# Performance work log

Measured on AMD Instinct MI355X. Metric: run time of the kernel, lower is better.

## Reference

```python
import jax, jax.numpy as jnp
import numpy as np

B, N, K = 4, 4096, 16
DP, DM = 64, 128
EPS = 1e-8


def setup_inputs() -> dict:
    key = jax.random.key(0)
    ks = jax.random.split(key, 32)
    g = lambda i, shape, fan: jax.random.normal(ks[i], shape, jnp.float32) / np.sqrt(fan)
    inp = {
        'xyz': jax.random.normal(ks[0], (B, N, 3), jnp.float32),
        'features': jax.random.normal(ks[1], (B, N, DP), jnp.float32),
        # fc1: d_points -> d_model
        'fc1_w': g(2, (DP, DM), DP), 'fc1_b': jnp.zeros((DM,), jnp.float32),
        # fc2: d_model -> d_points
        'fc2_w': g(3, (DM, DP), DM), 'fc2_b': jnp.zeros((DP,), jnp.float32),
        # fc_delta: Linear(3,DM) -> ReLU -> Linear(DM,DM)
        'd1_w': g(4, (3, DM), 3), 'd1_b': jnp.zeros((DM,), jnp.float32),
        'd2_w': g(5, (DM, DM), DM), 'd2_b': jnp.zeros((DM,), jnp.float32),
        # fc_gamma: Linear(DM,DM) -> ReLU -> Linear(DM,DM)
        'g1_w': g(6, (DM, DM), DM), 'g1_b': jnp.zeros((DM,), jnp.float32),
        'g2_w': g(7, (DM, DM), DM), 'g2_b': jnp.zeros((DM,), jnp.float32),
        # q/k/v projections, no bias
        'wq_w': g(8, (DM, DM), DM), 'wk_w': g(9, (DM, DM), DM), 'wv_w': g(10, (DM, DM), DM),
        # fc_sim: Linear(DM+1, DM)
        'sim_w': g(11, (DM + 1, DM), DM + 1), 'sim_b': jnp.zeros((DM,), jnp.float32),
    }
    return inp


def _gather(t, idx):
    # t: [B, N, C], idx: [B, N, K] -> [B, N, K, C]
    bidx = jnp.arange(t.shape[0])[:, None, None]
    return t[bidx, idx]


def reference(xyz, features, fc1_w, fc1_b, fc2_w, fc2_b, d1_w, d1_b, d2_w, d2_b,
              g1_w, g1_b, g2_w, g2_b, wq_w, wk_w, wv_w, sim_w, sim_b):
    # pairwise squared distances [B, N, N]
    sq = jnp.sum(xyz * xyz, axis=-1)
    dists = sq[:, :, None] + sq[:, None, :] - 2.0 * jnp.einsum('bnc,bmc->bnm', xyz, xyz)
    knn_idx = jnp.argsort(dists, axis=-1)[:, :, :K]            # [B, N, K]

    knn_xyz = _gather(xyz, knn_idx)                            # [B, N, K, 3]
    x = features @ fc1_w + fc1_b                               # [B, N, DM]
    q = x @ wq_w                                               # [B, N, DM]
    k = _gather(x @ wk_w, knn_idx)                             # [B, N, K, DM]
    v = _gather(x @ wv_w, knn_idx)                             # [B, N, K, DM]

    rel_pos = xyz[:, :, None, :] - knn_xyz                     # [B, N, K, 3]
    pos_enc = jax.nn.relu(rel_pos @ d1_w + d1_b) @ d2_w + d2_b # [B, N, K, DM]

    qe = q[:, :, None, :]                                      # [B, N, 1, DM]
    # torch cosine_similarity: dot / (max(||q||,eps) * max(||k||,eps))
    qn = jnp.maximum(jnp.linalg.norm(q, axis=-1), EPS)[:, :, None]
    kn = jnp.maximum(jnp.linalg.norm(k, axis=-1), EPS)
    sim = jnp.sum(qe * k, axis=-1) / (qn * kn)                 # [B, N, K]

    rel_qk = jnp.concatenate([sim[..., None], qe - k], axis=-1)  # [B, N, K, DM+1]
    rel_qk = rel_qk @ sim_w + sim_b                            # [B, N, K, DM]

    attn = jax.nn.relu((rel_qk + pos_enc) @ g1_w + g1_b) @ g2_w + g2_b
    attn = jax.nn.softmax(attn / np.sqrt(DM).astype(np.float32), axis=-2)  # over K

    res = jnp.einsum('bnkf,bnkf->bnf', attn, v + pos_enc)      # [B, N, DM]
    res = res @ fc2_w + fc2_b + features                       # [B, N, DP]
    return res, attn
```

## Files before the change

kernel.cpp:

```cpp
#include <hip/hip_runtime.h>
#include <hip/hip_bf16.h>

#define BB 4
#define NN 4096
#define KK 16
#define DP 64
#define DM 128
#define DMP 132
#define EPSF 1e-8f
#define OUT0N ((size_t)BB * NN * DP)

typedef unsigned short u16t;
typedef __attribute__((ext_vector_type(8))) short s8v;
typedef __attribute__((ext_vector_type(4))) float f4v;

__device__ int g_flag;

__device__ __forceinline__ float u2f(u16t u) {
    unsigned int x = ((unsigned int)u) << 16;
    return __uint_as_float(x);
}
__device__ __forceinline__ u16t f2u(float v) {
    __hip_bfloat16 h = __float2bfloat16(v);
    return *(u16t*)&h;
}

template<int DT> struct IO;
template<> struct IO<0> {
    static __device__ __forceinline__ float ld(const void* p, size_t i) { return ((const float*)p)[i]; }
    static __device__ __forceinline__ void ld4(const void* p, size_t i, float o[4]) {
        float4 v = *(const float4*)((const float*)p + i);
        o[0] = v.x; o[1] = v.y; o[2] = v.z; o[3] = v.w;
    }
    static __device__ __forceinline__ void st(void* p, size_t i, float v) { ((float*)p)[i] = v; }
};
template<> struct IO<1> {
    static __device__ __forceinline__ float ld(const void* p, size_t i) { return u2f(((const u16t*)p)[i]); }
    static __device__ __forceinline__ void ld4(const void* p, size_t i, float o[4]) {
        ushort4 v = *(const ushort4*)((const u16t*)p + i);
        o[0] = u2f(v.x); o[1] = u2f(v.y); o[2] = u2f(v.z); o[3] = u2f(v.w);
    }
    static __device__ __forceinline__ void st(void* p, size_t i, float v) { ((u16t*)p)[i] = f2u(v); }
};

__global__ __launch_bounds__(64) void detect_kernel(const void* feat) {
    const int tid = threadIdx.x;
    float x = u2f(((const u16t*)feat)[2 * tid]);
    float a = fabsf(x);
    bool sane = (x == 0.0f) || (a > 1e-4f && a < 50.0f);
    unsigned long long m = __ballot(sane);
    if (tid == 0) g_flag = (__popcll(m) >= 32) ? 1 : 0;
}

struct QkvSmem { float sf[DP]; float sx[DM]; };

template<int DT>
__device__ __forceinline__ void qkv_body(QkvSmem& s,
    const void* feat, const void* fc1_w, const void* fc1_b,
    const void* wq, const void* wk, const void* wv,
    float* __restrict__ qbuf, float* __restrict__ kbuf, float* __restrict__ vbuf)
{
    const int bn = blockIdx.x;
    const int tid = threadIdx.x;
    if (tid < DP) s.sf[tid] = IO<DT>::ld(feat, (size_t)bn * DP + tid);
    __syncthreads();
    float x = IO<DT>::ld(fc1_b, tid);
#pragma unroll 4
    for (int i = 0; i < DP; i++) x = fmaf(s.sf[i], IO<DT>::ld(fc1_w, i * DM + tid), x);
    s.sx[tid] = x;
    __syncthreads();
    float q = 0.f, k = 0.f, v = 0.f;
    for (int i0 = 0; i0 < DM; i0 += 4) {
        float4 xv = *(const float4*)&s.sx[i0];
        const float xs[4] = { xv.x, xv.y, xv.z, xv.w };
#pragma unroll
        for (int j = 0; j < 4; j++) {
            q = fmaf(xs[j], IO<DT>::ld(wq, (i0 + j) * DM + tid), q);
            k = fmaf(xs[j], IO<DT>::ld(wk, (i0 + j) * DM + tid), k);
            v = fmaf(xs[j], IO<DT>::ld(wv, (i0 + j) * DM + tid), v);
        }
    }
    qbuf[(size_t)bn * DM + tid] = q;
    kbuf[(size_t)bn * DM + tid] = k;
    vbuf[(size_t)bn * DM + tid] = v;
}

__global__ __launch_bounds__(128) void qkv_kernel(
    const void* feat, const void* fc1_w, const void* fc1_b,
    const void* wq, const void* wk, const void* wv,
    float* qbuf, float* kbuf, float* vbuf)
{
    __shared__ __align__(16) QkvSmem s;
    if (g_flag) qkv_body<1>(s, feat, fc1_w, fc1_b, wq, wk, wv, qbuf, kbuf, vbuf);
    else        qkv_body<0>(s, feat, fc1_w, fc1_b, wq, wk, wv, qbuf, kbuf, vbuf);
}

struct Qkv16Smem { float sf[16][DP]; float sx[16][DMP]; };

template<int DT>
__device__ __forceinline__ void qkv16_body(Qkv16Smem& s,
    const void* feat, const void* fc1_w, const void* fc1_b,
    const void* wq, const void* wk, const void* wv,
    float* __restrict__ qbuf, float* __restrict__ kbuf, float* __restrict__ vbuf)
{
    const int pnt0 = blockIdx.x << 4;
    const int tid = threadIdx.x;
    {
        const int r = tid >> 4, c4 = (tid & 15) << 2;
        float o[4];
        IO<DT>::ld4(feat, (size_t)(pnt0 + r) * DP + c4, o);
        s.sf[r][c4 + 0] = o[0]; s.sf[r][c4 + 1] = o[1];
        s.sf[r][c4 + 2] = o[2]; s.sf[r][c4 + 3] = o[3];
    }
    __syncthreads();
    const int c = tid & 127, h = tid >> 7;
    {
        float acc[8];
        const float fb = IO<DT>::ld(fc1_b, c);
#pragma unroll
        for (int pp = 0; pp < 8; pp++) acc[pp] = fb;
        for (int i = 0; i < DP; i++) {
            const float w = IO<DT>::ld(fc1_w, (size_t)i * DM + c);
#pragma unroll
            for (int pp = 0; pp < 8; pp++) acc[pp] = fmaf(s.sf[h * 8 + pp][i], w, acc[pp]);
        }
#pragma unroll
        for (int pp = 0; pp < 8; pp++) s.sx[h * 8 + pp][c] = acc[pp];
    }
    __syncthreads();
    {
        float aq[8], ak[8], av[8];
#pragma unroll
        for (int pp = 0; pp < 8; pp++) { aq[pp] = 0.f; ak[pp] = 0.f; av[pp] = 0.f; }
        for (int i0 = 0; i0 < DM; i0 += 4) {
            float x4[8][4];
#pragma unroll
            for (int pp = 0; pp < 8; pp++) {
                const float4 xv = *(const float4*)&s.sx[h * 8 + pp][i0];
                x4[pp][0] = xv.x; x4[pp][1] = xv.y; x4[pp][2] = xv.z; x4[pp][3] = xv.w;
            }
#pragma unroll
            for (int j = 0; j < 4; j++) {
                const float wqv = IO<DT>::ld(wq, (size_t)(i0 + j) * DM + c);
                const float wkv = IO<DT>::ld(wk, (size_t)(i0 + j) * DM + c);
                const float wvv = IO<DT>::ld(wv, (size_t)(i0 + j) * DM + c);
#pragma unroll
                for (int pp = 0; pp < 8; pp++) {
                    aq[pp] = fmaf(x4[pp][j], wqv, aq[pp]);
                    ak[pp] = fmaf(x4[pp][j], wkv, ak[pp]);
                    av[pp] = fmaf(x4[pp][j], wvv, av[pp]);
                }
            }
        }
#pragma unroll
        for (int pp = 0; pp < 8; pp++) {
            const size_t row = (size_t)(pnt0 + h * 8 + pp) * DM + c;
            qbuf[row] = aq[pp]; kbuf[row] = ak[pp]; vbuf[row] = av[pp];
        }
    }
}

__global__ __launch_bounds__(256) void qkv16_kernel(
    const void* feat, const void* fc1_w, const void* fc1_b,
    const void* wq, const void* wk, const void* wv,
    float* qbuf, float* kbuf, float* vbuf)
{
    __shared__ __align__(16) Qkv16Smem s;
    if (g_flag) qkv16_body<1>(s, feat, fc1_w, fc1_b, wq, wk, wv, qbuf, kbuf, vbuf);
    else        qkv16_body<0>(s, feat, fc1_w, fc1_b, wq, wk, wv, qbuf, kbuf, vbuf);
}

template<int DT>
__device__ __forceinline__ void knn_body(float4* __restrict__ sc,
    const void* xyz, int* dst, int dstride, void* dout, int in_out)
{
    if (in_out) {
        if (DT) { dst = (int*)((u16t*)dout + OUT0N); dstride = (KK * DM) / 2; }
        else    { dst = (int*)((float*)dout + OUT0N); dstride = KK * DM; }
    }
    const int b = blockIdx.x >> 9;
    const int tid = threadIdx.x;
    for (int j = tid; j < NN; j += 512) {
        float x = IO<DT>::ld(xyz, ((size_t)b * NN + j) * 3 + 0);
        float y = IO<DT>::ld(xyz, ((size_t)b * NN + j) * 3 + 1);
        float z = IO<DT>::ld(xyz, ((size_t)b * NN + j) * 3 + 2);
        float sq = __fadd_rn(__fadd_rn(__fmul_rn(x, x), __fmul_rn(y, y)), __fmul_rn(z, z));
        sc[j] = make_float4(x, y, z, sq);
    }
    __syncthreads();
    const int lane = tid & 63;
    const int wave = tid >> 6;
    const int r = ((blockIdx.x & 511) << 3) + wave;
    const float4 qc = sc[r];

    float d[KK];
    int id[KK];
#pragma unroll
    for (int t = 0; t < KK; t++) { d[t] = 3.4e38f; id[t] = 0x7fffffff; }

    for (int j = lane; j < NN; j += 64) {
        const float4 c = sc[j];
        const float dot = __fadd_rn(__fadd_rn(__fmul_rn(qc.x, c.x), __fmul_rn(qc.y, c.y)),
                                    __fmul_rn(qc.z, c.z));
        const float dist = __fsub_rn(__fadd_rn(qc.w, c.w), __fmul_rn(2.0f, dot));
        if (dist < d[KK - 1]) {
            float cd = dist; int ci = j;
#pragma unroll
            for (int t = 0; t < KK; t++) {
                const bool sw = (cd < d[t]);
                const float od = d[t]; const int oi = id[t];
                d[t]  = sw ? cd : d[t];
                id[t] = sw ? ci : id[t];
                cd = sw ? od : cd;
                ci = sw ? oi : ci;
            }
        }
    }

    const size_t base = (size_t)(b * NN + r) * (size_t)dstride;
#pragma unroll
    for (int t = 0; t < KK; t++) {
        float bd = d[0]; int bi = id[0];
#pragma unroll
        for (int off = 32; off >= 1; off >>= 1) {
            const float od = __shfl_xor(bd, off, 64);
            const int   oi = __shfl_xor(bi, off, 64);
            if (od < bd || (od == bd && oi < bi)) { bd = od; bi = oi; }
        }
        const bool win = (d[0] == bd) && (id[0] == bi);
        if (win) {
#pragma unroll
            for (int u = 0; u < KK - 1; u++) { d[u] = d[u + 1]; id[u] = id[u + 1]; }
            d[KK - 1] = 3.4e38f; id[KK - 1] = 0x7fffffff;
        }
        if (lane == t) dst[base + t] = bi;
    }
}

__global__ __launch_bounds__(512) void knn_kernel(
    const void* xyz, int* dst, int dstride, void* dout, int in_out)
{
    __shared__ __align__(16) float4 sc[NN];
    if (g_flag) knn_body<1>(sc, xyz, dst, dstride, dout, in_out);
    else        knn_body<0>(sc, xyz, dst, dstride, dout, in_out);
}

template<int DT>
__device__ __forceinline__ void gemm_tile(const float* __restrict__ IN,
                                          const void* __restrict__ W, int woff,
                                          int kg, int f0, float acc[4][4])
{
#pragma unroll
    for (int a = 0; a < 4; a++)
#pragma unroll
        for (int c = 0; c < 4; c++) acc[a][c] = 0.f;
    for (int i0 = 0; i0 < DM; i0 += 4) {
        float w[4][4];
#pragma unroll
        for (int j = 0; j < 4; j++) IO<DT>::ld4(W, (size_t)woff + (i0 + j) * DM + f0, w[j]);
#pragma unroll
        for (int kk = 0; kk < 4; kk++) {
            float4 x4 = *(const float4*)(IN + (kg * 4 + kk) * DMP + i0);
            const float xs[4] = { x4.x, x4.y, x4.z, x4.w };
#pragma unroll
            for (int ff = 0; ff < 4; ff++)
#pragma unroll
                for (int j = 0; j < 4; j++)
                    acc[kk][ff] = fmaf(xs[j], w[j][ff], acc[kk][ff]);
        }
    }
}

template<int DT>
__device__ __forceinline__ void wprep_body(const void* sim_w, const void* d2_w,
                                           const void* g1_w, const void* g2_w,
                                           u16t* __restrict__ wprep)
{
    const int m  = blockIdx.x >> 3;
    const int t  = blockIdx.x & 7;
    const int ks = threadIdx.x >> 6;
    const int lane = threadIdx.x & 63;
    const void* src = (m == 0) ? sim_w : (m == 1) ? d2_w : (m == 2) ? g1_w : g2_w;
    const int srcoff = (m == 0) ? DM : 0;
    u16t* hi = wprep + (size_t)m * 32768;
    u16t* lo = hi + 16384;
    const int c  = t * 16 + (lane & 15);
    const int k0 = ks * 32 + ((lane >> 4) << 3);
    s8v vh, vl;
#pragma unroll
    for (int j = 0; j < 8; j++) {
        const float x = IO<DT>::ld(src, (size_t)srcoff + (size_t)(k0 + j) * DM + c);
        const u16t h = f2u(x);
        vh[j] = (short)h;
        vl[j] = (short)f2u(x - u2f(h));
    }
    const size_t off = ((size_t)(t * 4 + ks) * 64 + lane) * 8;
    *(s8v*)(hi + off) = vh;
    *(s8v*)(lo + off) = vl;
}

__global__ __launch_bounds__(256) void wprep_kernel(
    const void* sim_w, const void* d2_w, const void* g1_w, const void* g2_w,
    u16t* wprep)
{
    if (g_flag) wprep_body<1>(sim_w, d2_w, g1_w, g2_w, wprep);
    else        wprep_body<0>(sim_w, d2_w, g1_w, g2_w, wprep);
}

template<int DT, int EPI>
__device__ __forceinline__ void mfma_gemm64(const float* __restrict__ IN,
                                            float* __restrict__ OUT,
                                            const u16t* __restrict__ wmat,
                                            const void* bias, const void* w0,
                                            const float* __restrict__ ssim)
{
    const int tid  = threadIdx.x;
    const int lane = tid & 63;
    const int wid  = tid >> 6;
    const int mt   = wid & 3;
    const int ch   = wid >> 2;
    const u16t* whi = wmat;
    const u16t* wlo = wmat + 16384;
    f4v acc[4] = { {0.f,0.f,0.f,0.f}, {0.f,0.f,0.f,0.f}, {0.f,0.f,0.f,0.f}, {0.f,0.f,0.f,0.f} };
    const float* ain = IN + (size_t)(mt * 16 + (lane & 15)) * DMP + ((lane >> 4) << 3);
#pragma unroll
    for (int ks = 0; ks < 4; ks++) {
        const float4 x0 = *(const float4*)(ain + ks * 32);
        const float4 x1 = *(const float4*)(ain + ks * 32 + 4);
        const float xs[8] = { x0.x, x0.y, x0.z, x0.w, x1.x, x1.y, x1.z, x1.w };
        s8v ahi, alo;
#pragma unroll
        for (int j = 0; j < 8; j++) {
            const u16t h = f2u(xs[j]);
            ahi[j] = (short)h;
            alo[j] = (short)f2u(xs[j] - u2f(h));
        }
#pragma unroll
        for (int t = 0; t < 4; t++) {
            const size_t off = ((size_t)((ch * 4 + t) * 4 + ks) * 64 + lane) * 8;
            const s8v bhi = *(const s8v*)(whi + off);
            const s8v blo = *(const s8v*)(wlo + off);
            acc[t] = __builtin_amdgcn_mfma_f32_16x16x32_bf16(ahi, bhi, acc[t], 0, 0, 0);
            acc[t] = __builtin_amdgcn_mfma_f32_16x16x32_bf16(ahi, blo, acc[t], 0, 0, 0);
            acc[t] = __builtin_amdgcn_mfma_f32_16x16x32_bf16(alo, bhi, acc[t], 0, 0, 0);
        }
    }
    const int r0 = (lane >> 4) * 4;
#pragma unroll
    for (int t = 0; t < 4; t++) {
        const int col = (ch * 4 + t) * 16 + (lane & 15);
        const float bv = IO<DT>::ld(bias, col);
        float w0v = 0.f;
        if constexpr (EPI == 2) w0v = IO<DT>::ld(w0, col);
#pragma unroll
        for (int r = 0; r < 4; r++) {
            const int row = mt * 16 + r0 + r;
            float v = acc[t][r] + bv;
            if constexpr (EPI == 2) v = fmaf(ssim[row], w0v, v);
            if constexpr (EPI == 1) v = fmaxf(v, 0.f);
            OUT[(size_t)row * DMP + col] = v;
        }
    }
}

struct AttnSmem4 {
    float KP[64 * DMP];
    float T0[64 * DMP];
    float T1[64 * DMP];
    float s_q[4 * DM], sres[4 * DM];
    float srp[64][3];
    float ssim[64], skn[64], sdot[64];
    float sqn[4];
    int sidx[64];
};

template<int DT>
__device__ __forceinline__ void attn4_body(AttnSmem4& s,
    const void* xyz, const void* feat,
    const void* fc2_w, const void* fc2_b,
    const void* d1_w, const void* d1_b, const void* d2_b,
    const void* g1_b, const void* g2_b,
    const void* sim_w, const void* sim_b,
    const float* __restrict__ qbuf, const float* __restrict__ kbuf,
    const float* __restrict__ vbuf,
    const int* __restrict__ knn, const u16t* __restrict__ wprep, void* dout)
{
    void* out0 = dout;
    void* out1 = DT ? (void*)((u16t*)dout + OUT0N) : (void*)((float*)dout + OUT0N);
    const int pnt0 = blockIdx.x << 2;
    const int b = pnt0 >> 12;
    const int tid = threadIdx.x;

    if (tid < 64) {
        int sv = knn[(size_t)(pnt0 + (tid >> 4)) * KK + (tid & 15)];
        sv = (sv < 0) ? 0 : (sv > NN - 1 ? NN - 1 : sv);
        s.sidx[tid] = sv;
    }
    __syncthreads();

    {
        const int p = tid >> 7, ff = tid & 127;
        s.s_q[tid] = qbuf[(size_t)(pnt0 + p) * DM + ff];
#pragma unroll
        for (int k = 0; k < KK; k++) {
            const int row = p * 16 + k;
            const int grow = (b << 12) + s.sidx[row];
            s.KP[row * DMP + ff] = kbuf[(size_t)grow * DM + ff];
        }
    }
    if (tid < 64) {
        const int grow = (b << 12) + s.sidx[tid];
        const int p = tid >> 4;
#pragma unroll
        for (int c = 0; c < 3; c++)
            s.srp[tid][c] = IO<DT>::ld(xyz, (size_t)(pnt0 + p) * 3 + c)
                          - IO<DT>::ld(xyz, (size_t)grow * 3 + c);
    }
    __syncthreads();

    {
        const int j = tid >> 3, g = tid & 7, p = j >> 4;
        float sk = 0.f, sd = 0.f, qq = 0.f;
#pragma unroll
        for (int i = 0; i < 16; i++) {
            const int ff = g * 16 + i;
            const float kv = s.KP[j * DMP + ff];
            const float qv = s.s_q[p * DM + ff];
            sk = fmaf(kv, kv, sk);
            sd = fmaf(qv, kv, sd);
            qq = fmaf(qv, qv, qq);
        }
#pragma unroll
        for (int off = 1; off <= 4; off <<= 1) {
            sk += __shfl_xor(sk, off, 64);
            sd += __shfl_xor(sd, off, 64);
            qq += __shfl_xor(qq, off, 64);
        }
        if (g == 0) {
            s.skn[j] = fmaxf(sqrtf(sk), EPSF);
            s.sdot[j] = sd;
            if ((j & 15) == 0) s.sqn[p] = fmaxf(sqrtf(qq), EPSF);
        }
    }
    __syncthreads();

    if (tid < 64) s.ssim[tid] = s.sdot[tid] / (s.sqn[tid >> 4] * s.skn[tid]);
    {
        const int p = tid >> 7, ff = tid & 127;
#pragma unroll
        for (int k = 0; k < KK; k++) {
            const int row = p * 16 + k;
            s.T0[row * DMP + ff] = s.s_q[p * DM + ff] - s.KP[row * DMP + ff];
        }
    }
    __syncthreads();

    mfma_gemm64<DT, 2>(s.T0, s.T1, wprep + 0 * 32768, sim_b, sim_w, s.ssim);
    __syncthreads();

    {
        const int p = tid >> 7, ff = tid & 127;
        const float w0 = IO<DT>::ld(d1_w, 0 * DM + ff), w1 = IO<DT>::ld(d1_w, 1 * DM + ff),
                    w2 = IO<DT>::ld(d1_w, 2 * DM + ff);
        const float hb = IO<DT>::ld(d1_b, ff);
#pragma unroll
        for (int k = 0; k < KK; k++) {
            const int row = p * 16 + k;
            const float h = fmaf(s.srp[row][2], w2,
                            fmaf(s.srp[row][1], w1, fmaf(s.srp[row][0], w0, hb)));
            s.T0[row * DMP + ff] = fmaxf(h, 0.f);
        }
    }
    __syncthreads();

    mfma_gemm64<DT, 0>(s.T0, s.KP, wprep + 1 * 32768, d2_b, nullptr, nullptr);
    __syncthreads();

    {
        const int p = tid >> 7, ff = tid & 127;
#pragma unroll
        for (int k = 0; k < KK; k++) {
            const int row = p * 16 + k;
            s.T0[row * DMP + ff] = s.T1[row * DMP + ff] + s.KP[row * DMP + ff];
        }
    }
    __syncthreads();

    mfma_gemm64<DT, 1>(s.T0, s.T1, wprep + 2 * 32768, g1_b, nullptr, nullptr);
    __syncthreads();

    mfma_gemm64<DT, 0>(s.T1, s.T0, wprep + 3 * 32768, g2_b, nullptr, nullptr);
    __syncthreads();

    {
        const int p = tid >> 7, ff = tid & 127;
        const float sq128 = 11.31370849898476f;
        float tv[KK];
        float mx = -3.4e38f;
#pragma unroll
        for (int k = 0; k < KK; k++) {
            tv[k] = s.T0[(p * 16 + k) * DMP + ff] / sq128;
            mx = fmaxf(mx, tv[k]);
        }
        float ssum = 0.f;
#pragma unroll
        for (int k = 0; k < KK; k++) { tv[k] = expf(tv[k] - mx); ssum += tv[k]; }
        float rf = 0.f;
#pragma unroll
        for (int k = 0; k < KK; k++) {
            const float a = tv[k] / ssum;
            IO<DT>::st(out1, ((size_t)(pnt0 + p) * KK + k) * DM + ff, a);
            const int row = p * 16 + k;
            const int grow = (b << 12) + s.sidx[row];
            rf = fmaf(a, vbuf[(size_t)grow * DM + ff] + s.KP[row * DMP + ff], rf);
        }
        s.sres[tid] = rf;
    }
    __syncthreads();

    if (tid < 256) {
        const int p = tid >> 6, c = tid & 63;
        float o = 0.f;
        for (int i = 0; i < DM; i++) o = fmaf(s.sres[p * DM + i], IO<DT>::ld(fc2_w, (size_t)i * DP + c), o);
        o = o + IO<DT>::ld(fc2_b, c) + IO<DT>::ld(feat, (size_t)(pnt0 + p) * DP + c);
        IO<DT>::st(out0, (size_t)(pnt0 + p) * DP + c, o);
    }
}

__global__ __launch_bounds__(512) void attn4_kernel(
    const void* xyz, const void* feat,
    const void* fc2_w, const void* fc2_b,
    const void* d1_w, const void* d1_b, const void* d2_b,
    const void* g1_b, const void* g2_b,
    const void* sim_w, const void* sim_b,
    const float* qbuf, const float* kbuf, const float* vbuf,
    const int* knn, const u16t* wprep, void* dout)
{
    __shared__ __align__(16) AttnSmem4 s;
    if (g_flag)
        attn4_body<1>(s, xyz, feat, fc2_w, fc2_b, d1_w, d1_b, d2_b, g1_b, g2_b,
                      sim_w, sim_b, qbuf, kbuf, vbuf, knn, wprep, dout);
    else
        attn4_body<0>(s, xyz, feat, fc2_w, fc2_b, d1_w, d1_b, d2_b, g1_b, g2_b,
                      sim_w, sim_b, qbuf, kbuf, vbuf, knn, wprep, dout);
}

template<bool FUSED> struct AttnSmem {
    float Kb[KK * DMP], Vb[KK * DMP], PE[KK * DMP], T0[KK * DMP], T1[KK * DMP];
    float s_q[DM], sres[DM];
    float SF[FUSED ? 17 * DP : 1];
    float X[FUSED ? 17 * DMP : 1];
    float srp[KK][3];
    float ssim[KK], skn[KK], sdot[KK];
    float sqn;
    int sidx[KK];
};

template<int DT, bool FUSED>
__device__ __forceinline__ void attn_body(AttnSmem<FUSED>& s,
    const void* xyz, const void* feat,
    const void* fc1_w, const void* fc1_b, const void* fc2_w, const void* fc2_b,
    const void* d1_w, const void* d1_b, const void* d2_w, const void* d2_b,
    const void* g1_w, const void* g1_b, const void* g2_w, const void* g2_b,
    const void* sim_w, const void* sim_b,
    const void* wq, const void* wk, const void* wv,
    const float* __restrict__ qbuf, const float* __restrict__ kbuf, const float* __restrict__ vbuf,
    const int* knn, int knn_stride, int knn_in_out, void* dout)
{
    void* out0 = dout;
    void* out1 = DT ? (void*)((u16t*)dout + OUT0N) : (void*)((float*)dout + OUT0N);
    if (knn_in_out) {
        if (DT) { knn = (const int*)((const u16t*)dout + OUT0N); knn_stride = (KK * DM) / 2; }
        else    { knn = (const int*)((const float*)dout + OUT0N); knn_stride = KK * DM; }
    }

    const int bn = blockIdx.x;
    const int b = bn >> 12;
    const int tid = threadIdx.x;
    const int f = tid;
    const int f0 = (tid & 31) * 4;
    const int kg = tid >> 5;

    if (tid < KK) {
        int sv = knn[(size_t)bn * knn_stride + tid];
        sv = (sv < 0) ? 0 : (sv > NN - 1 ? NN - 1 : sv);
        s.sidx[tid] = sv;
    }
    __syncthreads();

    if constexpr (FUSED) {
        for (int idx = tid; idx < 17 * DP; idx += 128) {
            const int r = idx >> 6, c = idx & 63;
            const int row = (r < KK) ? ((b << 12) + s.sidx[r]) : bn;
            s.SF[idx] = IO<DT>::ld(feat, (size_t)row * DP + c);
        }
        __syncthreads();
        float xacc[17];
        const float fb = IO<DT>::ld(fc1_b, tid);
#pragma unroll
        for (int r = 0; r < 17; r++) xacc[r] = fb;
        for (int i = 0; i < DP; i++) {
            const float w = IO<DT>::ld(fc1_w, i * DM + tid);
#pragma unroll
            for (int r = 0; r < 17; r++) xacc[r] = fmaf(s.SF[r * DP + i], w, xacc[r]);
        }
#pragma unroll
        for (int r = 0; r < 17; r++) s.X[r * DMP + tid] = xacc[r];
        __syncthreads();
        {
            float a2[4][4];
            gemm_tile<DT>(s.X, wk, 0, kg, f0, a2);
#pragma unroll
            for (int kk = 0; kk < 4; kk++)
                *(float4*)&s.Kb[(kg * 4 + kk) * DMP + f0] =
                    make_float4(a2[kk][0], a2[kk][1], a2[kk][2], a2[kk][3]);
            gemm_tile<DT>(s.X, wv, 0, kg, f0, a2);
#pragma unroll
            for (int kk = 0; kk < 4; kk++)
                *(float4*)&s.Vb[(kg * 4 + kk) * DMP + f0] =
                    make_float4(a2[kk][0], a2[kk][1], a2[kk][2], a2[kk][3]);
        }
        {
            float qv = 0.f;
            for (int i0 = 0; i0 < DM; i0 += 4) {
                float4 x4 = *(const float4*)&s.X[16 * DMP + i0];
                const float xs[4] = { x4.x, x4.y, x4.z, x4.w };
#pragma unroll
                for (int j = 0; j < 4; j++)
                    qv = fmaf(xs[j], IO<DT>::ld(wq, (i0 + j) * DM + tid), qv);
            }
            s.s_q[tid] = qv;
        }
    } else {
        s.s_q[f] = qbuf[(size_t)bn * DM + f];
#pragma unroll
        for (int k = 0; k < KK; k++) {
            const int row = (b << 12) + s.sidx[k];
            s.Kb[k * DMP + f] = kbuf[(size_t)row * DM + f];
            s.Vb[k * DMP + f] = vbuf[(size_t)row * DM + f];
        }
    }
    if (tid < KK) {
        const int row = (b << 12) + s.sidx[tid];
#pragma unroll
        for (int c = 0; c < 3; c++)
            s.srp[tid][c] = IO<DT>::ld(xyz, (size_t)bn * 3 + c) - IO<DT>::ld(xyz, (size_t)row * 3 + c);
    }
    __syncthreads();

    if (tid < KK) {
        float sk = 0.f, sd = 0.f;
        for (int i = 0; i < DM; i++) {
            float v2 = s.Kb[tid * DMP + i];
            sk = fmaf(v2, v2, sk);
            sd = fmaf(s.s_q[i], v2, sd);
        }
        s.skn[tid] = fmaxf(sqrtf(sk), EPSF);
        s.sdot[tid] = sd;
    } else if (tid == KK) {
        float sqq = 0.f;
        for (int i = 0; i < DM; i++) { float v2 = s.s_q[i]; sqq = fmaf(v2, v2, sqq); }
        s.sqn = fmaxf(sqrtf(sqq), EPSF);
    }
    __syncthreads();
    if (tid < KK) s.ssim[tid] = s.sdot[tid] / (s.sqn * s.skn[tid]);
#pragma unroll
    for (int k = 0; k < KK; k++) s.T0[k * DMP + f] = s.s_q[f] - s.Kb[k * DMP + f];
    __syncthreads();

    float acc[4][4];

    gemm_tile<DT>(s.T0, sim_w, DM, kg, f0, acc);
    {
        float w0f[4], sbf[4];
        IO<DT>::ld4(sim_w, f0, w0f);
        IO<DT>::ld4(sim_b, f0, sbf);
#pragma unroll
        for (int kk = 0; kk < 4; kk++) {
            float sm = s.ssim[kg * 4 + kk];
            float4 o;
            o.x = fmaf(sm, w0f[0], acc[kk][0]) + sbf[0];
            o.y = fmaf(sm, w0f[1], acc[kk][1]) + sbf[1];
            o.z = fmaf(sm, w0f[2], acc[kk][2]) + sbf[2];
            o.w = fmaf(sm, w0f[3], acc[kk][3]) + sbf[3];
            *(float4*)&s.T1[(kg * 4 + kk) * DMP + f0] = o;
        }
    }
    __syncthreads();

    {
        float w0 = IO<DT>::ld(d1_w, 0 * DM + f), w1 = IO<DT>::ld(d1_w, 1 * DM + f),
              w2 = IO<DT>::ld(d1_w, 2 * DM + f);
        float hb = IO<DT>::ld(d1_b, f);
#pragma unroll
        for (int k = 0; k < KK; k++) {
            float h = fmaf(s.srp[k][2], w2, fmaf(s.srp[k][1], w1, fmaf(s.srp[k][0], w0, hb)));
            s.T0[k * DMP + f] = fmaxf(h, 0.f);
        }
    }
    __syncthreads();

    gemm_tile<DT>(s.T0, d2_w, 0, kg, f0, acc);
    {
        float bf[4];
        IO<DT>::ld4(d2_b, f0, bf);
#pragma unroll
        for (int kk = 0; kk < 4; kk++)
            *(float4*)&s.PE[(kg * 4 + kk) * DMP + f0] =
                make_float4(acc[kk][0] + bf[0], acc[kk][1] + bf[1],
                            acc[kk][2] + bf[2], acc[kk][3] + bf[3]);
    }
    __syncthreads();

#pragma unroll
    for (int kk = 0; kk < 4; kk++) {
        const int row = (kg * 4 + kk) * DMP + f0;
        float4 a4 = *(const float4*)&s.T1[row];
        float4 p4 = *(const float4*)&s.PE[row];
        *(float4*)&s.T0[row] = make_float4(a4.x + p4.x, a4.y + p4.y, a4.z + p4.z, a4.w + p4.w);
    }
    __syncthreads();

    gemm_tile<DT>(s.T0, g1_w, 0, kg, f0, acc);
    {
        float bf[4];
        IO<DT>::ld4(g1_b, f0, bf);
#pragma unroll
        for (int kk = 0; kk < 4; kk++)
            *(float4*)&s.T1[(kg * 4 + kk) * DMP + f0] =
                make_float4(fmaxf(acc[kk][0] + bf[0], 0.f), fmaxf(acc[kk][1] + bf[1], 0.f),
                            fmaxf(acc[kk][2] + bf[2], 0.f), fmaxf(acc[kk][3] + bf[3], 0.f));
    }
    __syncthreads();

    gemm_tile<DT>(s.T1, g2_w, 0, kg, f0, acc);
    {
        float bf[4];
        IO<DT>::ld4(g2_b, f0, bf);
#pragma unroll
        for (int kk = 0; kk < 4; kk++)
            *(float4*)&s.T0[(kg * 4 + kk) * DMP + f0] =
                make_float4(acc[kk][0] + bf[0], acc[kk][1] + bf[1],
                            acc[kk][2] + bf[2], acc[kk][3] + bf[3]);
    }
    __syncthreads();

    {
        const float sq128 = 11.31370849898476f;
        float tv[KK];
        float m = -3.4e38f;
#pragma unroll
        for (int k = 0; k < KK; k++) { tv[k] = s.T0[k * DMP + f] / sq128; m = fmaxf(m, tv[k]); }
        float ssum = 0.f;
#pragma unroll
        for (int k = 0; k < KK; k++) { tv[k] = expf(tv[k] - m); ssum += tv[k]; }
        float rf = 0.f;
#pragma unroll
        for (int k = 0; k < KK; k++) {
            float a = tv[k] / ssum;
            IO<DT>::st(out1, ((size_t)bn * KK + k) * DM + f, a);
            rf = fmaf(a, s.Vb[k * DMP + f] + s.PE[k * DMP + f], rf);
        }
        s.sres[f] = rf;
    }
    __syncthreads();

    if (tid < DP) {
        float o = 0.f;
        for (int i = 0; i < DM; i++) o = fmaf(s.sres[i], IO<DT>::ld(fc2_w, i * DP + tid), o);
        o = o + IO<DT>::ld(fc2_b, tid) + IO<DT>::ld(feat, (size_t)bn * DP + tid);
        IO<DT>::st(out0, (size_t)bn * DP + tid, o);
    }
}

template<bool FUSED>
__global__ __launch_bounds__(128) void attn_kernel(
    const void* xyz, const void* feat,
    const void* fc1_w, const void* fc1_b, const void* fc2_w, const void* fc2_b,
    const void* d1_w, const void* d1_b, const void* d2_w, const void* d2_b,
    const void* g1_w, const void* g1_b, const void* g2_w, const void* g2_b,
    const void* sim_w, const void* sim_b,
    const void* wq, const void* wk, const void* wv,
    const float* qbuf, const float* kbuf, const float* vbuf,
    const int* knn, int knn_stride, int knn_in_out, void* dout)
{
    __shared__ __align__(16) AttnSmem<FUSED> s;
    if (g_flag)
        attn_body<1, FUSED>(s, xyz, feat, fc1_w, fc1_b, fc2_w, fc2_b, d1_w, d1_b, d2_w, d2_b,
                            g1_w, g1_b, g2_w, g2_b, sim_w, sim_b, wq, wk, wv,
                            qbuf, kbuf, vbuf, knn, knn_stride, knn_in_out, dout);
    else
        attn_body<0, FUSED>(s, xyz, feat, fc1_w, fc1_b, fc2_w, fc2_b, d1_w, d1_b, d2_w, d2_b,
                            g1_w, g1_b, g2_w, g2_b, sim_w, sim_b, wq, wk, wv,
                            qbuf, kbuf, vbuf, knn, knn_stride, knn_in_out, dout);
}

extern "C" void kernel_launch(void* const* d_in, const int* in_sizes, int n_in,
                              void* d_out, int out_size, void* d_ws, size_t ws_size,
                              hipStream_t stream)
{
    const void* xyz   = d_in[0];
    const void* feat  = d_in[1];
    const void* fc1_w = d_in[2];
    const void* fc1_b = d_in[3];
    const void* fc2_w = d_in[4];
    const void* fc2_b = d_in[5];
    const void* d1_w  = d_in[6];
    const void* d1_b  = d_in[7];
    const void* d2_w  = d_in[8];
    const void* d2_b  = d_in[9];
    const void* g1_w  = d_in[10];
    const void* g1_b  = d_in[11];
    const void* g2_w  = d_in[12];
    const void* g2_b  = d_in[13];
    const void* wq_w  = d_in[14];
    const void* wk_w  = d_in[15];
    const void* wv_w  = d_in[16];
    const void* sim_w = d_in[17];
    const void* sim_b = d_in[18];

    detect_kernel<<<1, 64, 0, stream>>>(feat);

    const size_t need_qkv = (size_t)3 * BB * NN * DM * sizeof(float);
    const size_t need_knn = (size_t)BB * NN * KK * sizeof(int);
    const size_t need_wp  = (size_t)4 * 2 * 16384 * sizeof(u16t);

    if (ws_size >= need_qkv + need_knn + need_wp && d_ws != nullptr) {
        float* qbuf  = (float*)d_ws;
        float* kbuf  = qbuf + (size_t)BB * NN * DM;
        float* vbuf  = kbuf + (size_t)BB * NN * DM;
        int*   knn   = (int*)(vbuf + (size_t)BB * NN * DM);
        u16t*  wprep = (u16t*)(knn + (size_t)BB * NN * KK);
        qkv16_kernel<<<(BB * NN) / 16, 256, 0, stream>>>(feat, fc1_w, fc1_b, wq_w, wk_w, wv_w,
                                                         qbuf, kbuf, vbuf);
        knn_kernel<<<BB * 512, 512, 0, stream>>>(xyz, knn, KK, d_out, 0);
        wprep_kernel<<<32, 256, 0, stream>>>(sim_w, d2_w, g1_w, g2_w, wprep);
        attn4_kernel<<<(BB * NN) / 4, 512, 0, stream>>>(
            xyz, feat, fc2_w, fc2_b, d1_w, d1_b, d2_b, g1_b, g2_b, sim_w, sim_b,
            qbuf, kbuf, vbuf, knn, wprep, d_out);
    } else if (ws_size >= need_qkv + need_knn && d_ws != nullptr) {
        float* qbuf = (float*)d_ws;
        float* kbuf = qbuf + (size_t)BB * NN * DM;
        float* vbuf = kbuf + (size_t)BB * NN * DM;
        int*   knn  = (int*)(vbuf + (size_t)BB * NN * DM);
        qkv_kernel<<<BB * NN, DM, 0, stream>>>(feat, fc1_w, fc1_b, wq_w, wk_w, wv_w, qbuf, kbuf, vbuf);
        knn_kernel<<<BB * 512, 512, 0, stream>>>(xyz, knn, KK, d_out, 0);
        attn_kernel<false><<<BB * NN, DM, 0, stream>>>(
            xyz, feat, fc1_w, fc1_b, fc2_w, fc2_b, d1_w, d1_b, d2_w, d2_b,
            g1_w, g1_b, g2_w, g2_b, sim_w, sim_b, wq_w, wk_w, wv_w,
            qbuf, kbuf, vbuf, knn, KK, 0, d_out);
    } else if (ws_size >= need_knn && d_ws != nullptr) {
        int* knn = (int*)d_ws;
        knn_kernel<<<BB * 512, 512, 0, stream>>>(xyz, knn, KK, d_out, 0);
        attn_kernel<true><<<BB * NN, DM, 0, stream>>>(
            xyz, feat, fc1_w, fc1_b, fc2_w, fc2_b, d1_w, d1_b, d2_w, d2_b,
            g1_w, g1_b, g2_w, g2_b, sim_w, sim_b, wq_w, wk_w, wv_w,
            nullptr, nullptr, nullptr, knn, KK, 0, d_out);
    } else {
        knn_kernel<<<BB * 512, 512, 0, stream>>>(xyz, nullptr, 0, d_out, 1);
        attn_kernel<true><<<BB * NN, DM, 0, stream>>>(
            xyz, feat, fc1_w, fc1_b, fc2_w, fc2_b, d1_w, d1_b, d2_w, d2_b,
            g1_w, g1_b, g2_w, g2_b, sim_w, sim_b, wq_w, wk_w, wv_w,
            nullptr, nullptr, nullptr, nullptr, 0, 1, d_out);
    }
}
```

Baseline: 705.8 us.

## Switch attention kernel to one point per 128-thread block with pre-split bf16 LDS operands

```diff
diff --git a/kernel.cpp b/kernel.cpp
--- a/kernel.cpp
+++ b/kernel.cpp
@@ -7,6 +7,7 @@
 #define DP 64
 #define DM 128
 #define DMP 132
+#define SPITCH 264
 #define EPSF 1e-8f
 #define OUT0N ((size_t)BB * NN * DP)
 
@@ -23,6 +24,12 @@
 __device__ __forceinline__ u16t f2u(float v) {
     __hip_bfloat16 h = __float2bfloat16(v);
     return *(u16t*)&h;
+}
+__device__ __forceinline__ void splitf(float x, u16t& h, u16t& l) {
+    const unsigned xb = __float_as_uint(x);
+    h = (u16t)(xb >> 16);
+    const float hf = __uint_as_float(xb & 0xffff0000u);
+    l = (u16t)(__float_as_uint(x - hf) >> 16);
 }
 
 template<int DT> struct IO;
@@ -307,37 +314,20 @@
     else        wprep_body<0>(sim_w, d2_w, g1_w, g2_w, wprep);
 }
 
-template<int DT, int EPI>
-__device__ __forceinline__ void mfma_gemm64(const float* __restrict__ IN,
-                                            float* __restrict__ OUT,
-                                            const u16t* __restrict__ wmat,
-                                            const void* bias, const void* w0,
-                                            const float* __restrict__ ssim)
-{
-    const int tid  = threadIdx.x;
-    const int lane = tid & 63;
-    const int wid  = tid >> 6;
-    const int mt   = wid & 3;
-    const int ch   = wid >> 2;
+__device__ __forceinline__ void mfma_core(const u16t* __restrict__ SP,
+                                          const u16t* __restrict__ wmat,
+                                          int lane, int wid, f4v acc[4])
+{
     const u16t* whi = wmat;
     const u16t* wlo = wmat + 16384;
-    f4v acc[4] = { {0.f,0.f,0.f,0.f}, {0.f,0.f,0.f,0.f}, {0.f,0.f,0.f,0.f}, {0.f,0.f,0.f,0.f} };
-    const float* ain = IN + (size_t)(mt * 16 + (lane & 15)) * DMP + ((lane >> 4) << 3);
+    const u16t* ar = SP + (size_t)(lane & 15) * SPITCH + ((lane >> 4) << 3);
 #pragma unroll
     for (int ks = 0; ks < 4; ks++) {
-        const float4 x0 = *(const float4*)(ain + ks * 32);
-        const float4 x1 = *(const float4*)(ain + ks * 32 + 4);
-        const float xs[8] = { x0.x, x0.y, x0.z, x0.w, x1.x, x1.y, x1.z, x1.w };
-        s8v ahi, alo;
-#pragma unroll
-        for (int j = 0; j < 8; j++) {
-            const u16t h = f2u(xs[j]);
-            ahi[j] = (short)h;
-            alo[j] = (short)f2u(xs[j] - u2f(h));
-        }
+        const s8v ahi = *(const s8v*)(ar + ks * 32);
+        const s8v alo = *(const s8v*)(ar + 128 + ks * 32);
 #pragma unroll
         for (int t = 0; t < 4; t++) {
-            const size_t off = ((size_t)((ch * 4 + t) * 4 + ks) * 64 + lane) * 8;
+            const size_t off = ((size_t)((wid * 4 + t) * 4 + ks) * 64 + lane) * 8;
             const s8v bhi = *(const s8v*)(whi + off);
             const s8v blo = *(const s8v*)(wlo + off);
             acc[t] = __builtin_amdgcn_mfma_f32_16x16x32_bf16(ahi, bhi, acc[t], 0, 0, 0);
@@ -345,37 +335,22 @@
             acc[t] = __builtin_amdgcn_mfma_f32_16x16x32_bf16(alo, bhi, acc[t], 0, 0, 0);
         }
     }
-    const int r0 = (lane >> 4) * 4;
-#pragma unroll
-    for (int t = 0; t < 4; t++) {
-        const int col = (ch * 4 + t) * 16 + (lane & 15);
-        const float bv = IO<DT>::ld(bias, col);
-        float w0v = 0.f;
-        if constexpr (EPI == 2) w0v = IO<DT>::ld(w0, col);
-#pragma unroll
-        for (int r = 0; r < 4; r++) {
-            const int row = mt * 16 + r0 + r;
-            float v = acc[t][r] + bv;
-            if constexpr (EPI == 2) v = fmaf(ssim[row], w0v, v);
-            if constexpr (EPI == 1) v = fmaxf(v, 0.f);
-            OUT[(size_t)row * DMP + col] = v;
-        }
-    }
-}
-
-struct AttnSmem4 {
-    float KP[64 * DMP];
-    float T0[64 * DMP];
-    float T1[64 * DMP];
-    float s_q[4 * DM], sres[4 * DM];
-    float srp[64][3];
-    float ssim[64], skn[64], sdot[64];
-    float sqn[4];
-    int sidx[64];
+}
+
+struct AttnSmemS {
+    float KF[KK * DMP];
+    float T1[KK * DMP];
+    u16t  SP[KK * SPITCH];
+    float s_q[DM];
+    float sred[DM];
+    float sp2[DM];
+    float srp[KK][3];
+    float ssim[KK];
+    int   sidx[KK];
 };
 
 template<int DT>
-__device__ __forceinline__ void attn4_body(AttnSmem4& s,
+__device__ __forceinline__ void attn_sp_body(AttnSmemS& s,
     const void* xyz, const void* feat,
     const void* fc2_w, const void* fc2_b,
     const void* d1_w, const void* d1_b, const void* d2_b,
@@ -387,48 +362,48 @@
 {
     void* out0 = dout;
     void* out1 = DT ? (void*)((u16t*)dout + OUT0N) : (void*)((float*)dout + OUT0N);
-    const int pnt0 = blockIdx.x << 2;
-    const int b = pnt0 >> 12;
+    const int bn = blockIdx.x;
+    const int b = bn >> 12;
     const int tid = threadIdx.x;
-
-    if (tid < 64) {
-        int sv = knn[(size_t)(pnt0 + (tid >> 4)) * KK + (tid & 15)];
+    const int f = tid;
+    const int lane = tid & 63;
+    const int wid = tid >> 6;
+
+    if (tid < KK) {
+        int sv = knn[(size_t)bn * KK + tid];
         sv = (sv < 0) ? 0 : (sv > NN - 1 ? NN - 1 : sv);
         s.sidx[tid] = sv;
     }
     __syncthreads();
 
-    {
-        const int p = tid >> 7, ff = tid & 127;
-        s.s_q[tid] = qbuf[(size_t)(pnt0 + p) * DM + ff];
+    float vreg[KK];
+    {
+        s.s_q[f] = qbuf[(size_t)bn * DM + f];
 #pragma unroll
         for (int k = 0; k < KK; k++) {
-            const int row = p * 16 + k;
-            const int grow = (b << 12) + s.sidx[row];
-            s.KP[row * DMP + ff] = kbuf[(size_t)grow * DM + ff];
-        }
-    }
-    if (tid < 64) {
+            const int grow = (b << 12) + s.sidx[k];
+            s.KF[k * DMP + f] = kbuf[(size_t)grow * DM + f];
+            vreg[k] = vbuf[(size_t)grow * DM + f];
+        }
+    }
+    if (tid < KK) {
         const int grow = (b << 12) + s.sidx[tid];
-        const int p = tid >> 4;
 #pragma unroll
         for (int c = 0; c < 3; c++)
-            s.srp[tid][c] = IO<DT>::ld(xyz, (size_t)(pnt0 + p) * 3 + c)
-                          - IO<DT>::ld(xyz, (size_t)grow * 3 + c);
-    }
-    __syncthreads();
-
-    {
-        const int j = tid >> 3, g = tid & 7, p = j >> 4;
+            s.srp[tid][c] = IO<DT>::ld(xyz, (size_t)bn * 3 + c) - IO<DT>::ld(xyz, (size_t)grow * 3 + c);
+    }
+    __syncthreads();
+
+    {
+        const int j = tid >> 3, g = tid & 7;
         float sk = 0.f, sd = 0.f, qq = 0.f;
 #pragma unroll
-        for (int i = 0; i < 16; i++) {
-            const int ff = g * 16 + i;
-            const float kv = s.KP[j * DMP + ff];
-            const float qv = s.s_q[p * DM + ff];
-            sk = fmaf(kv, kv, sk);
-            sd = fmaf(qv, kv, sd);
-            qq = fmaf(qv, qv, qq);
+        for (int i4 = 0; i4 < 16; i4 += 4) {
+            const float4 kv = *(const float4*)&s.KF[j * DMP + g * 16 + i4];
+            const float4 qv = *(const float4*)&s.s_q[g * 16 + i4];
+            sk = fmaf(kv.x, kv.x, fmaf(kv.y, kv.y, fmaf(kv.z, kv.z, fmaf(kv.w, kv.w, sk))));
+            sd = fmaf(qv.x, kv.x, fmaf(qv.y, kv.y, fmaf(qv.z, kv.z, fmaf(qv.w, kv.w, sd))));
+            qq = fmaf(qv.x, qv.x, fmaf(qv.y, qv.y, fmaf(qv.z, qv.z, fmaf(qv.w, qv.w, qq))));
         }
 #pragma unroll
         for (int off = 1; off <= 4; off <<= 1) {
@@ -437,97 +412,177 @@
             qq += __shfl_xor(qq, off, 64);
         }
         if (g == 0) {
-            s.skn[j] = fmaxf(sqrtf(sk), EPSF);
-            s.sdot[j] = sd;
-            if ((j & 15) == 0) s.sqn[p] = fmaxf(sqrtf(qq), EPSF);
-        }
-    }
-    __syncthreads();
-
-    if (tid < 64) s.ssim[tid] = s.sdot[tid] / (s.sqn[tid >> 4] * s.skn[tid]);
-    {
-        const int p = tid >> 7, ff = tid & 127;
-#pragma unroll
-        for (int k = 0; k < KK; k++) {
-            const int row = p * 16 + k;
-            s.T0[row * DMP + ff] = s.s_q[p * DM + ff] - s.KP[row * DMP + ff];
-        }
-    }
-    __syncthreads();
-
-    mfma_gemm64<DT, 2>(s.T0, s.T1, wprep + 0 * 32768, sim_b, sim_w, s.ssim);
-    __syncthreads();
-
-    {
-        const int p = tid >> 7, ff = tid & 127;
-        const float w0 = IO<DT>::ld(d1_w, 0 * DM + ff), w1 = IO<DT>::ld(d1_w, 1 * DM + ff),
-                    w2 = IO<DT>::ld(d1_w, 2 * DM + ff);
-        const float hb = IO<DT>::ld(d1_b, ff);
-#pragma unroll
-        for (int k = 0; k < KK; k++) {
-            const int row = p * 16 + k;
-            const float h = fmaf(s.srp[row][2], w2,
-                            fmaf(s.srp[row][1], w1, fmaf(s.srp[row][0], w0, hb)));
-            s.T0[row * DMP + ff] = fmaxf(h, 0.f);
-        }
-    }
-    __syncthreads();
-
-    mfma_gemm64<DT, 0>(s.T0, s.KP, wprep + 1 * 32768, d2_b, nullptr, nullptr);
-    __syncthreads();
-
-    {
-        const int p = tid >> 7, ff = tid & 127;
-#pragma unroll
-        for (int k = 0; k < KK; k++) {
-            const int row = p * 16 + k;
-            s.T0[row * DMP + ff] = s.T1[row * DMP + ff] + s.KP[row * DMP + ff];
-        }
-    }
-    __syncthreads();
-
-    mfma_gemm64<DT, 1>(s.T0, s.T1, wprep + 2 * 32768, g1_b, nullptr, nullptr);
-    __syncthreads();
-
-    mfma_gemm64<DT, 0>(s.T1, s.T0, wprep + 3 * 32768, g2_b, nullptr, nullptr);
-    __syncthreads();
-
-    {
-        const int p = tid >> 7, ff = tid & 127;
-        const float sq128 = 11.31370849898476f;
+            const float qn = fmaxf(sqrtf(qq), EPSF);
+            const float kn = fmaxf(sqrtf(sk), EPSF);
+            s.ssim[j] = sd / (qn * kn);
+        }
+    }
+    {
+        const int r = tid & 15, c0 = (tid >> 4) << 4;
+        u16t* hp = &s.SP[r * SPITCH + c0];
+        u16t* lp = hp + 128;
+#pragma unroll
+        for (int j4 = 0; j4 < 16; j4 += 4) {
+            const float4 kv = *(const float4*)&s.KF[r * DMP + c0 + j4];
+            const float4 qv = *(const float4*)&s.s_q[c0 + j4];
+            ushort4 hv, lv;
+            splitf(qv.x - kv.x, hv.x, lv.x);
+            splitf(qv.y - kv.y, hv.y, lv.y);
+            splitf(qv.z - kv.z, hv.z, lv.z);
+            splitf(qv.w - kv.w, hv.w, lv.w);
+            *(ushort4*)(hp + j4) = hv;
+            *(ushort4*)(lp + j4) = lv;
+        }
+    }
+    __syncthreads();
+
+    {
+        f4v acc[4] = { {0,0,0,0},{0,0,0,0},{0,0,0,0},{0,0,0,0} };
+        mfma_core(s.SP, wprep + 0 * 32768, lane, wid, acc);
+        const int r0 = (lane >> 4) * 4;
+#pragma unroll
+        for (int t = 0; t < 4; t++) {
+            const int col = (wid * 4 + t) * 16 + (lane & 15);
+            const float bv = IO<DT>::ld(sim_b, col);
+            const float w0v = IO<DT>::ld(sim_w, col);
+#pragma unroll
+            for (int r = 0; r < 4; r++)
+                s.T1[(size_t)(r0 + r) * DMP + col] = fmaf(s.ssim[r0 + r], w0v, acc[t][r] + bv);
+        }
+    }
+    __syncthreads();
+
+    {
+        const int r = tid & 15, c0 = (tid >> 4) << 4;
+        const float rx = s.srp[r][0], ry = s.srp[r][1], rz = s.srp[r][2];
+        u16t* hp = &s.SP[r * SPITCH + c0];
+        u16t* lp = hp + 128;
+#pragma unroll
+        for (int j4 = 0; j4 < 16; j4 += 4) {
+            float w0[4], w1[4], w2[4], bb[4];
+            IO<DT>::ld4(d1_w, (size_t)0 * DM + c0 + j4, w0);
+            IO<DT>::ld4(d1_w, (size_t)1 * DM + c0 + j4, w1);
+            IO<DT>::ld4(d1_w, (size_t)2 * DM + c0 + j4, w2);
+            IO<DT>::ld4(d1_b, c0 + j4, bb);
+            ushort4 hv, lv;
+#pragma unroll
+            for (int jj = 0; jj < 4; jj++) {
+                const float h = fmaxf(fmaf(rz, w2[jj], fmaf(ry, w1[jj], fmaf(rx, w0[jj], bb[jj]))), 0.f);
+                u16t hs, ls; splitf(h, hs, ls);
+                ((u16t*)&hv)[jj] = hs; ((u16t*)&lv)[jj] = ls;
+            }
+            *(ushort4*)(hp + j4) = hv;
+            *(ushort4*)(lp + j4) = lv;
+        }
+    }
+    __syncthreads();
+
+    {
+        f4v acc[4] = { {0,0,0,0},{0,0,0,0},{0,0,0,0},{0,0,0,0} };
+        mfma_core(s.SP, wprep + 1 * 32768, lane, wid, acc);
+        const int r0 = (lane >> 4) * 4;
+#pragma unroll
+        for (int t = 0; t < 4; t++) {
+            const int col = (wid * 4 + t) * 16 + (lane & 15);
+            const float bv = IO<DT>::ld(d2_b, col);
+#pragma unroll
+            for (int r = 0; r < 4; r++)
+                s.KF[(size_t)(r0 + r) * DMP + col] = acc[t][r] + bv;
+        }
+    }
+    __syncthreads();
+
+    {
+        const int r = tid & 15, c0 = (tid >> 4) << 4;
+        u16t* hp = &s.SP[r * SPITCH + c0];
+        u16t* lp = hp + 128;
+#pragma unroll
+        for (int j4 = 0; j4 < 16; j4 += 4) {
+            const float4 t4 = *(const float4*)&s.T1[r * DMP + c0 + j4];
+            const float4 p4 = *(const float4*)&s.KF[r * DMP + c0 + j4];
+            ushort4 hv, lv;
+            splitf(t4.x + p4.x, hv.x, lv.x);
+            splitf(t4.y + p4.y, hv.y, lv.y);
+            splitf(t4.z + p4.z, hv.z, lv.z);
+            splitf(t4.w + p4.w, hv.w, lv.w);
+            *(ushort4*)(hp + j4) = hv;
+            *(ushort4*)(lp + j4) = lv;
+        }
+    }
+    __syncthreads();
+
+    {
+        f4v acc[4] = { {0,0,0,0},{0,0,0,0},{0,0,0,0},{0,0,0,0} };
+        mfma_core(s.SP, wprep + 2 * 32768, lane, wid, acc);
+        __syncthreads();
+        const int r0 = (lane >> 4) * 4;
+#pragma unroll
+        for (int t = 0; t < 4; t++) {
+            const int col = (wid * 4 + t) * 16 + (lane & 15);
+            const float bv = IO<DT>::ld(g1_b, col);
+#pragma unroll
+            for (int r = 0; r < 4; r++) {
+                const float v = fmaxf(acc[t][r] + bv, 0.f);
+                u16t hs, ls; splitf(v, hs, ls);
+                s.SP[(size_t)(r0 + r) * SPITCH + col] = hs;
+                s.SP[(size_t)(r0 + r) * SPITCH + 128 + col] = ls;
+            }
+        }
+    }
+    __syncthreads();
+
+    {
+        f4v acc[4] = { {0,0,0,0},{0,0,0,0},{0,0,0,0},{0,0,0,0} };
+        mfma_core(s.SP, wprep + 3 * 32768, lane, wid, acc);
+        const int r0 = (lane >> 4) * 4;
+#pragma unroll
+        for (int t = 0; t < 4; t++) {
+            const int col = (wid * 4 + t) * 16 + (lane & 15);
+            const float bv = IO<DT>::ld(g2_b, col);
+#pragma unroll
+            for (int r = 0; r < 4; r++)
+                s.T1[(size_t)(r0 + r) * DMP + col] = acc[t][r] + bv;
+        }
+    }
+    __syncthreads();
+
+    {
+        const float inv = 0.08838834764831843f;
         float tv[KK];
         float mx = -3.4e38f;
 #pragma unroll
+        for (int k = 0; k < KK; k++) { tv[k] = s.T1[k * DMP + f] * inv; mx = fmaxf(mx, tv[k]); }
+        float ssum = 0.f;
+#pragma unroll
+        for (int k = 0; k < KK; k++) { tv[k] = __expf(tv[k] - mx); ssum += tv[k]; }
+        const float rs = 1.0f / ssum;
+        float rf = 0.f;
+#pragma unroll
         for (int k = 0; k < KK; k++) {
-            tv[k] = s.T0[(p * 16 + k) * DMP + ff] / sq128;
-            mx = fmaxf(mx, tv[k]);
-        }
-        float ssum = 0.f;
-#pragma unroll
-        for (int k = 0; k < KK; k++) { tv[k] = expf(tv[k] - mx); ssum += tv[k]; }
-        float rf = 0.f;
-#pragma unroll
-        for (int k = 0; k < KK; k++) {
-            const float a = tv[k] / ssum;
-            IO<DT>::st(out1, ((size_t)(pnt0 + p) * KK + k) * DM + ff, a);
-            const int row = p * 16 + k;
-            const int grow = (b << 12) + s.sidx[row];
-            rf = fmaf(a, vbuf[(size_t)grow * DM + ff] + s.KP[row * DMP + ff], rf);
-        }
-        s.sres[tid] = rf;
-    }
-    __syncthreads();
-
-    if (tid < 256) {
-        const int p = tid >> 6, c = tid & 63;
+            const float a = tv[k] * rs;
+            IO<DT>::st(out1, ((size_t)bn * KK + k) * DM + f, a);
+            rf = fmaf(a, vreg[k] + s.KF[k * DMP + f], rf);
+        }
+        s.sred[f] = rf;
+    }
+    __syncthreads();
+
+    {
+        const int c = tid & 63, hh = tid >> 6;
         float o = 0.f;
-        for (int i = 0; i < DM; i++) o = fmaf(s.sres[p * DM + i], IO<DT>::ld(fc2_w, (size_t)i * DP + c), o);
-        o = o + IO<DT>::ld(fc2_b, c) + IO<DT>::ld(feat, (size_t)(pnt0 + p) * DP + c);
-        IO<DT>::st(out0, (size_t)(pnt0 + p) * DP + c, o);
-    }
-}
-
-__global__ __launch_bounds__(512) void attn4_kernel(
+        for (int i = hh * 64; i < hh * 64 + 64; i++)
+            o = fmaf(s.sred[i], IO<DT>::ld(fc2_w, (size_t)i * DP + c), o);
+        s.sp2[tid] = o;
+    }
+    __syncthreads();
+    if (tid < DP) {
+        float o = s.sp2[tid] + s.sp2[tid + 64];
+        o = o + IO<DT>::ld(fc2_b, tid) + IO<DT>::ld(feat, (size_t)bn * DP + tid);
+        IO<DT>::st(out0, (size_t)bn * DP + tid, o);
+    }
+}
+
+__global__ __launch_bounds__(128) void attn_sp_kernel(
     const void* xyz, const void* feat,
     const void* fc2_w, const void* fc2_b,
     const void* d1_w, const void* d1_b, const void* d2_b,
@@ -536,13 +591,13 @@
     const float* qbuf, const float* kbuf, const float* vbuf,
     const int* knn, const u16t* wprep, void* dout)
 {
-    __shared__ __align__(16) AttnSmem4 s;
+    __shared__ __align__(16) AttnSmemS s;
     if (g_flag)
-        attn4_body<1>(s, xyz, feat, fc2_w, fc2_b, d1_w, d1_b, d2_b, g1_b, g2_b,
-                      sim_w, sim_b, qbuf, kbuf, vbuf, knn, wprep, dout);
+        attn_sp_body<1>(s, xyz, feat, fc2_w, fc2_b, d1_w, d1_b, d2_b, g1_b, g2_b,
+                        sim_w, sim_b, qbuf, kbuf, vbuf, knn, wprep, dout);
     else
-        attn4_body<0>(s, xyz, feat, fc2_w, fc2_b, d1_w, d1_b, d2_b, g1_b, g2_b,
-                      sim_w, sim_b, qbuf, kbuf, vbuf, knn, wprep, dout);
+        attn_sp_body<0>(s, xyz, feat, fc2_w, fc2_b, d1_w, d1_b, d2_b, g1_b, g2_b,
+                        sim_w, sim_b, qbuf, kbuf, vbuf, knn, wprep, dout);
 }
 
 template<bool FUSED> struct AttnSmem {
@@ -835,7 +890,7 @@
                                                          qbuf, kbuf, vbuf);
         knn_kernel<<<BB * 512, 512, 0, stream>>>(xyz, knn, KK, d_out, 0);
         wprep_kernel<<<32, 256, 0, stream>>>(sim_w, d2_w, g1_w, g2_w, wprep);
-        attn4_kernel<<<(BB * NN) / 4, 512, 0, stream>>>(
+        attn_sp_kernel<<<BB * NN, 128, 0, stream>>>(
             xyz, feat, fc2_w, fc2_b, d1_w, d1_b, d2_b, g1_b, g2_b, sim_w, sim_b,
             qbuf, kbuf, vbuf, knn, wprep, d_out);
     } else if (ws_size >= need_qkv + need_knn && d_ws != nullptr) {
```

New measurement: 645.0 us. 1.09x faster.
